# Optimization experiments

Measured on AMD Instinct MI355X. Metric: run time of the kernel, lower is better.

Reference implementation:

```python
import jax, jax.numpy as jnp
import numpy as np

B, L, H, W = 4, 5000, 256, 256
C_IN, DIM_LOI, N_PTS0, N_PTS1, DIM_FC, N_OUT_LINE = 256, 128, 32, 8, 1024, 2500
SCALE = N_PTS0 // N_PTS1  # MaxPool1d kernel/stride


def setup_inputs() -> dict:
    key = jax.random.key(0)
    ks = jax.random.split(key, 8)
    feature = jax.random.normal(ks[0], (B, C_IN, H, W), jnp.float32)
    # line endpoints in pixel coords of the 256x256 feature map
    lines = jax.random.uniform(ks[1], (B, L, 2, 2), jnp.float32) * (H - 1)
    s = lambda fan: 1.0 / np.sqrt(fan)
    fc1_w = (jax.random.normal(ks[2], (DIM_LOI, C_IN), jnp.float32) * s(C_IN))
    fc1_b = jnp.zeros((DIM_LOI,), jnp.float32)
    w1 = jax.random.normal(ks[3], (DIM_LOI * N_PTS1, DIM_FC), jnp.float32) * s(DIM_LOI * N_PTS1)
    b1 = jnp.zeros((DIM_FC,), jnp.float32)
    w2 = jax.random.normal(ks[4], (DIM_FC, DIM_FC), jnp.float32) * s(DIM_FC)
    b2 = jnp.zeros((DIM_FC,), jnp.float32)
    w3 = jax.random.normal(ks[5], (DIM_FC, 4), jnp.float32) * s(DIM_FC)
    b3 = jnp.zeros((4,), jnp.float32)
    return dict(feature=feature, lines=lines, fc1_w=fc1_w, fc1_b=fc1_b,
                w1=w1, b1=b1, w2=w2, b2=b2, w3=w3, b3=b3)


def reference(feature, lines, fc1_w, fc1_b, w1, b1, w2, b2, w3, b3):
    # fc1: 1x1 conv  [B,C_IN,H,W] -> [B,DIM_LOI,H,W]
    x = jnp.einsum('bchw,oc->bohw', feature, fc1_w) + fc1_b[None, :, None, None]

    # sample N_PTS0 points along each line (lerp between endpoints), minus 0.5
    lam = jnp.linspace(0.0, 1.0, N_PTS0, dtype=feature.dtype)[None, None, :, None]
    p = lines[:, :, 0:1, :] * lam + lines[:, :, 1:2, :] * (1.0 - lam) - 0.5  # [B,L,P,2]
    px, py = p[..., 0], p[..., 1]  # px indexes H (rows), py indexes W (cols)
    px0 = jnp.clip(jnp.floor(px), 0.0, H - 1.0)
    py0 = jnp.clip(jnp.floor(py), 0.0, W - 1.0)
    px1 = jnp.clip(px0 + 1.0, 0.0, H - 1.0)
    py1 = jnp.clip(py0 + 1.0, 0.0, W - 1.0)
    ix0, iy0 = px0.astype(jnp.int32), py0.astype(jnp.int32)
    ix1, iy1 = px1.astype(jnp.int32), py1.astype(jnp.int32)
    idx00 = ix0 * W + iy0
    idx10 = ix1 * W + iy0
    idx01 = ix0 * W + iy1
    idx11 = ix1 * W + iy1
    w00 = (px1 - px) * (py1 - py)
    w10 = (px - px0) * (py1 - py)
    w01 = (px1 - px) * (py - py0)
    w11 = (px - px0) * (py - py0)

    def gather_one(fmap, i00, i10, i01, i11, g00, g10, g01, g11):
        f = fmap.reshape(DIM_LOI, H * W)
        g = lambda idx: f[:, idx.reshape(-1)].reshape(DIM_LOI, L, N_PTS0)
        return g(i00) * g00 + g(i10) * g10 + g(i01) * g01 + g(i11) * g11

    xp = jax.vmap(gather_one)(x, idx00, idx10, idx01, idx11, w00, w10, w01, w11)
    # xp: [B, DIM_LOI, L, N_PTS0] -> maxpool along points -> [B, DIM_LOI, L, N_PTS1]
    xp = xp.reshape(B, DIM_LOI, L, N_PTS1, SCALE).max(-1)
    # reshape like torch: [N, DIM_LOI, N_PTS1] -> [N, DIM_LOI*N_PTS1] (channel-major)
    feat = xp.transpose(0, 2, 1, 3).reshape(B, L, DIM_LOI * N_PTS1)

    # fc2 MLP -> 4 logits
    h = jax.nn.relu(feat @ w1 + b1)
    h = jax.nn.relu(h @ w2 + b2)
    logits = h @ w3 + b3  # [B, L, 4]
    s = jax.nn.softmax(logits, axis=-1)

    # threshold conditions
    keep = ((s[..., 1] > 0.25) | (s[..., 2] > 0.25) | (s[..., 3] > 0.25)) & (s[..., 0] < 0.25)

    def select(p0, s0, m):
        cnt = m.sum()
        key = jnp.where(m, jnp.argmax(s0, -1), -1)  # masked-out get -1 -> sorted last
        order = jnp.argsort(-key)  # stable desc sort of argmax class
        idx = order[jnp.arange(N_OUT_LINE) % jnp.maximum(cnt, 1)]
        lo = jnp.where(cnt > 0, p0[idx], 0.0)
        so = jnp.where(cnt > 0, s0[idx], 0.0)
        return lo, so

    lines_out, score_out = jax.vmap(select)(lines, s, keep)
    return lines_out, score_out, s
```

## Files before the change

### kernel.cpp

```cpp
#include <hip/hip_runtime.h>
#include <cstdint>
#include <cstddef>

#define B_     4
#define L_     5000
#define H_     256
#define W_     256
#define HW_    65536
#define CIN_   256
#define DLOI_  128
#define NPTS0_ 32
#define NPTS1_ 8
#define DFC_   1024
#define NOUT_  2500
#define M_     (B_*L_)
#define MPAD_  20096
#define NBAND_ 157

typedef _Float16 f16;
typedef _Float16 f16x4 __attribute__((ext_vector_type(4)));
typedef _Float16 f16x8 __attribute__((ext_vector_type(8)));
typedef float    f32x4 __attribute__((ext_vector_type(4)));

__device__ __forceinline__ void gload16(const void* g, void* l) {
  __builtin_amdgcn_global_load_lds(
      (const __attribute__((address_space(1))) void*)g,
      (__attribute__((address_space(3))) void*)l, 16, 0, 0);
}

__global__ __launch_bounds__(256) void k_wsplit(const float* __restrict__ src,
                                                f16* __restrict__ h,
                                                f16* __restrict__ l) {
  int i = (blockIdx.x * 256 + threadIdx.x) * 4;
  float4 v = *(const float4*)(src + i);
  f16 h0 = (f16)v.x, h1 = (f16)v.y, h2 = (f16)v.z, h3 = (f16)v.w;
  *(f16x4*)(h + i) = (f16x4){h0, h1, h2, h3};
  *(f16x4*)(l + i) = (f16x4){(f16)(v.x - (float)h0), (f16)(v.y - (float)h1),
                             (f16)(v.z - (float)h2), (f16)(v.w - (float)h3)};
}

__global__ __launch_bounds__(1024) void k_order(const float* __restrict__ lines,
                                                int* __restrict__ perm) {
  __shared__ int hist[64];
  __shared__ int off[64];
  const int b = blockIdx.x;
  const int t = threadIdx.x;
  if (t < 64) hist[t] = 0;
  __syncthreads();
  int mycell[5];
  #pragma unroll
  for (int i = 0; i < 5; i++) {
    const int l = t * 5 + i;
    int cell = -1;
    if (l < L_) {
      const float* ln = lines + (size_t)(b * L_ + l) * 4;
      float mx = 0.5f * (ln[0] + ln[2]);
      float my = 0.5f * (ln[1] + ln[3]);
      int cx = min(max((int)mx, 0), 255) >> 5;
      int cy = min(max((int)my, 0), 255) >> 5;
      cell = (cx & 1) | ((cy & 1) << 1) | ((cx & 2) << 1) | ((cy & 2) << 2)
           | ((cx & 4) << 2) | ((cy & 4) << 3);
      atomicAdd(&hist[cell], 1);
    }
    mycell[i] = cell;
  }
  __syncthreads();
  if (t == 0) {
    int s = 0;
    for (int c = 0; c < 64; c++) { off[c] = s; s += hist[c]; }
  }
  __syncthreads();
  #pragma unroll
  for (int i = 0; i < 5; i++) {
    if (mycell[i] >= 0) {
      int slot = atomicAdd(&off[mycell[i]], 1);
      perm[b * L_ + slot] = t * 5 + i;
    }
  }
}

__global__ __launch_bounds__(256) void k_conv_mfma(const float* __restrict__ fin,
                                                   const f16* __restrict__ wh,
                                                   const f16* __restrict__ wl,
                                                   const float* __restrict__ bias,
                                                   float* __restrict__ xout) {
  __shared__ f16 lds[16384];
  const int t = threadIdx.x;
  const int P0 = blockIdx.x * 128;
  const int b  = P0 >> 16;
  const int ph0 = P0 & 65535;
  const int lane = t & 63, wave = t >> 6;
  const int quad = lane >> 4, lo = lane & 15;
  const int wm = wave >> 1, wn = wave & 1;

  const int c_base = (t & 7) * 4;
  const int p = (t >> 3) * 4;
  const size_t fbase = (size_t)b * CIN_ * HW_ + (size_t)ph0 + p;

  const int srow = t >> 2;
  const int skb  = (t & 3) * 16;
  const char* gBh = (const char*)wh + (size_t)srow * 512 + skb;
  const char* gBl = (const char*)wl + (size_t)srow * 512 + skb;
  char* ldsB = (char*)lds + t * 16;

  f32x4 acc[4][4];
  #pragma unroll
  for (int mt = 0; mt < 4; mt++)
    #pragma unroll
    for (int nt = 0; nt < 4; nt++) acc[mt][nt] = (f32x4){0.f, 0.f, 0.f, 0.f};

  float4 av[4], nv[4];
  #pragma unroll
  for (int j = 0; j < 4; j++)
    av[j] = *(const float4*)(fin + fbase + (size_t)(c_base + j) * HW_);

  for (int kc = 0; kc < 8; kc++) {
    const size_t bko = (size_t)kc * 64;
    gload16(gBh + bko,         ldsB + 16384);
    gload16(gBh + 32768 + bko, ldsB + 16384 + 4096);
    gload16(gBl + bko,         ldsB + 24576);
    gload16(gBl + 32768 + bko, ldsB + 24576 + 4096);

    #pragma unroll
    for (int i = 0; i < 4; i++) {
      f16 hh[4], ll[4];
      #pragma unroll
      for (int j = 0; j < 4; j++) {
        float v = ((const float*)&av[j])[i];
        hh[j] = (f16)v;
        ll[j] = (f16)(v - (float)hh[j]);
      }
      *(f16x4*)(&lds[(p + i) * 32 + c_base])        = (f16x4){hh[0], hh[1], hh[2], hh[3]};
      *(f16x4*)(&lds[4096 + (p + i) * 32 + c_base]) = (f16x4){ll[0], ll[1], ll[2], ll[3]};
    }
    __syncthreads();

    if (kc < 7) {
      #pragma unroll
      for (int j = 0; j < 4; j++)
        nv[j] = *(const float4*)(fin + fbase + (size_t)((kc + 1) * 32 + c_base + j) * HW_);
    }

    f16x8 ah[4], al[4], bh4[4], bl4[4];
    #pragma unroll
    for (int mt = 0; mt < 4; mt++) {
      int row = wm * 64 + mt * 16 + lo;
      ah[mt] = *(const f16x8*)(&lds[row * 32 + quad * 8]);
      al[mt] = *(const f16x8*)(&lds[4096 + row * 32 + quad * 8]);
    }
    #pragma unroll
    for (int nt = 0; nt < 4; nt++) {
      int row = wn * 64 + nt * 16 + lo;
      bh4[nt] = *(const f16x8*)(&lds[8192 + row * 32 + quad * 8]);
      bl4[nt] = *(const f16x8*)(&lds[12288 + row * 32 + quad * 8]);
    }
    #pragma unroll
    for (int mt = 0; mt < 4; mt++)
      #pragma unroll
      for (int nt = 0; nt < 4; nt++) {
        acc[mt][nt] = __builtin_amdgcn_mfma_f32_16x16x32_f16(ah[mt], bh4[nt], acc[mt][nt], 0, 0, 0);
        acc[mt][nt] = __builtin_amdgcn_mfma_f32_16x16x32_f16(ah[mt], bl4[nt], acc[mt][nt], 0, 0, 0);
        acc[mt][nt] = __builtin_amdgcn_mfma_f32_16x16x32_f16(al[mt], bh4[nt], acc[mt][nt], 0, 0, 0);
      }
    __syncthreads();
    #pragma unroll
    for (int j = 0; j < 4; j++) av[j] = nv[j];
  }

  #pragma unroll
  for (int nt = 0; nt < 4; nt++) {
    int col = wn * 64 + nt * 16 + lo;
    float bv = bias[col];
    #pragma unroll
    for (int mt = 0; mt < 4; mt++) {
      int rowb = P0 + wm * 64 + mt * 16 + quad * 4;
      #pragma unroll
      for (int r = 0; r < 4; r++)
        xout[(size_t)(rowb + r) * DLOI_ + col] = acc[mt][nt][r] + bv;
    }
  }
}

__global__ __launch_bounds__(128) void k_sample(const float* __restrict__ x,
                                                const float* __restrict__ lines,
                                                const int* __restrict__ perm,
                                                f16* __restrict__ fh,
                                                f16* __restrict__ fl) {
  __shared__ int4   s_off[NPTS0_];
  __shared__ float4 s_wt [NPTS0_];
  const int blk0 = blockIdx.x;
  const int s = (blk0 & 7) * (M_ / 8) + (blk0 >> 3);
  const int b = s / L_;
  const int row = b * L_ + perm[s];
  const int c = threadIdx.x;
  const float* ln = lines + (size_t)row * 4;

  if (c < NPTS0_) {
    const float e0x = ln[0], e0y = ln[1], e1x = ln[2], e1y = ln[3];
    const int i = c;
    float lam = (float)i * (1.0f / 31.0f);
    float px = e0x * lam + e1x * (1.f - lam) - 0.5f;
    float py = e0y * lam + e1y * (1.f - lam) - 0.5f;
    float px0 = fminf(fmaxf(floorf(px), 0.f), 255.f);
    float py0 = fminf(fmaxf(floorf(py), 0.f), 255.f);
    float px1 = fminf(px0 + 1.f, 255.f);
    float py1 = fminf(py0 + 1.f, 255.f);
    int ix0 = (int)px0, iy0 = (int)py0, ix1 = (int)px1, iy1 = (int)py1;
    s_wt[i]  = make_float4((px1 - px) * (py1 - py),
                           (px - px0) * (py1 - py),
                           (px1 - px) * (py - py0),
                           (px - px0) * (py - py0));
    s_off[i] = make_int4((ix0 * W_ + iy0) * (DLOI_ * 4),
                         (ix1 * W_ + iy0) * (DLOI_ * 4),
                         (ix0 * W_ + iy1) * (DLOI_ * 4),
                         (ix1 * W_ + iy1) * (DLOI_ * 4));
  }
  __syncthreads();

  const char* xbc = (const char*)(x + (size_t)b * HW_ * DLOI_) + c * 4;
  f16x8 vh, vl;
  for (int q = 0; q < NPTS1_; q++) {
    float m = -1e30f;
    #pragma unroll
    for (int r = 0; r < 4; r++) {
      const int i = q * 4 + r;
      const int4   o = s_off[i];
      const float4 w = s_wt[i];
      float v = w.x * *(const float*)(xbc + o.x)
              + w.y * *(const float*)(xbc + o.y)
              + w.z * *(const float*)(xbc + o.z)
              + w.w * *(const float*)(xbc + o.w);
      m = fmaxf(m, v);
    }
    f16 h = (f16)m;
    vh[q] = h;
    vl[q] = (f16)(m - (float)h);
  }
  *(f16x8*)(fh + (size_t)row * DFC_ + c * 8) = vh;
  *(f16x8*)(fl + (size_t)row * DFC_ + c * 8) = vl;
}

__global__ __launch_bounds__(256) void k_tsplit(const float* __restrict__ Wsrc,
                                                f16* __restrict__ Th,
                                                f16* __restrict__ Tl) {
  __shared__ float tile[32][33];
  const int bj = blockIdx.x, bi = blockIdx.y;
  const int tx = threadIdx.x & 31, ty = threadIdx.x >> 5;
  #pragma unroll
  for (int r = ty; r < 32; r += 8)
    tile[r][tx] = Wsrc[(size_t)(bi * 32 + r) * 1024 + bj * 32 + tx];
  __syncthreads();
  #pragma unroll
  for (int r = ty; r < 32; r += 8) {
    float v = tile[tx][r];
    f16 h = (f16)v;
    size_t o = (size_t)(bj * 32 + r) * 1024 + bi * 32 + tx;
    Th[o] = h;
    Tl[o] = (f16)(v - (float)h);
  }
}

#define BKT_    32
#define NTT_    (DFC_/BKT_)
#define SLOT_B_ 49152
#define AH_O_   0
#define AL_O_   8192
#define BH_O_   16384
#define BL_O_   32768

template <bool SPLIT_OUT>
__global__ __launch_bounds__(512, 2) void k_gemm_f16x3(
    const f16* __restrict__ Ah, const f16* __restrict__ Al,
    const f16* __restrict__ Bh, const f16* __restrict__ Bl,
    const float* __restrict__ bias,
    f16* __restrict__ Oh, f16* __restrict__ Ol,
    const float* __restrict__ w3, float* __restrict__ part) {
  __shared__ f16 lds[3 * SLOT_B_ / 2];
  char* ldsc = (char*)lds;

  const int orig = blockIdx.x;
  const int xcd = orig & 7, bidx = orig >> 3;
  const int qq = 628 >> 3, rr = 628 & 7;
  const int wg = (xcd < rr ? xcd * (qq + 1) : rr * (qq + 1) + (xcd - rr) * qq) + bidx;
  const int band = wg >> 2;
  const int nb   = wg & 3;
  const int r0 = band * 128;
  const int n0 = nb * 256;

  const int t = threadIdx.x;
  const int lane = t & 63, wave = t >> 6;
  const int quad = lane >> 4, lo = lane & 15;
  const int wm = wave >> 2, wn = wave & 3;

  const uint32_t usA  = (uint32_t)t ^ (((uint32_t)t >> 3) & 7);
  const uint32_t uB1  = (uint32_t)t + 512u;
  const uint32_t usB1 = uB1 ^ ((uB1 >> 3) & 7);
  const size_t sA  = (size_t)(usA  >> 2) * 2048 + (size_t)(usA  & 3) * 16;
  const size_t sB1 = (size_t)(usB1 >> 2) * 2048 + (size_t)(usB1 & 3) * 16;

  const char* gAh  = (const char*)Ah + (size_t)r0 * 2048 + sA;
  const char* gAl  = (const char*)Al + (size_t)r0 * 2048 + sA;
  const char* gBh0 = (const char*)Bh + (size_t)n0 * 2048 + sA;
  const char* gBh1 = (const char*)Bh + (size_t)n0 * 2048 + sB1;
  const char* gBl0 = (const char*)Bl + (size_t)n0 * 2048 + sA;
  const char* gBl1 = (const char*)Bl + (size_t)n0 * 2048 + sB1;

  const int dAh  = AH_O_ + t * 16;
  const int dAl  = AL_O_ + t * 16;
  const int dBh0 = BH_O_ + t * 16;
  const int dBh1 = BH_O_ + 8192 + t * 16;
  const int dBl0 = BL_O_ + t * 16;
  const int dBl1 = BL_O_ + 8192 + t * 16;

  int roffA[4], roffB[4];
  #pragma unroll
  for (int mt = 0; mt < 4; mt++) {
    int r = wm * 64 + mt * 16 + lo;
    roffA[mt] = (((r * 4 + quad) ^ ((r >> 1) & 7)) << 4);
  }
  #pragma unroll
  for (int nt = 0; nt < 4; nt++) {
    int r = wn * 64 + nt * 16 + lo;
    roffB[nt] = (((r * 4 + quad) ^ ((r >> 1) & 7)) << 4);
  }

  f32x4 acc[4][4];
  #pragma unroll
  for (int mt = 0; mt < 4; mt++)
    #pragma unroll
    for (int nt = 0; nt < 4; nt++) acc[mt][nt] = (f32x4){0.f, 0.f, 0.f, 0.f};

  gload16(gAh,        ldsc + dAh);
  gload16(gAl,        ldsc + dAl);
  gload16(gBh0,       ldsc + dBh0);
  gload16(gBh1,       ldsc + dBh1);
  gload16(gBl0,       ldsc + dBl0);
  gload16(gBl1,       ldsc + dBl1);
  gload16(gAh  + 64,  ldsc + SLOT_B_ + dAh);
  gload16(gAl  + 64,  ldsc + SLOT_B_ + dAl);
  gload16(gBh0 + 64,  ldsc + SLOT_B_ + dBh0);
  gload16(gBh1 + 64,  ldsc + SLOT_B_ + dBh1);
  gload16(gBl0 + 64,  ldsc + SLOT_B_ + dBl0);
  gload16(gBl1 + 64,  ldsc + SLOT_B_ + dBl1);
  asm volatile("s_waitcnt vmcnt(6)" ::: "memory");
  __builtin_amdgcn_s_barrier();

  int cur = 0, stg = 2;
  for (int tt = 0; tt < NTT_; ++tt) {
    const char* sc = ldsc + cur * SLOT_B_;
    char* sw = ldsc + stg * SLOT_B_;
    const size_t go = (size_t)tt * 64 + 128;
    const bool pf = (tt + 2 < NTT_);

    if (pf) {
      gload16(gAh  + go, sw + dAh);
      gload16(gAl  + go, sw + dAl);
      gload16(gBh0 + go, sw + dBh0);
      gload16(gBh1 + go, sw + dBh1);
      gload16(gBl0 + go, sw + dBl0);
      gload16(gBl1 + go, sw + dBl1);
    }

    f16x8 ah[4], bh[4], al[4], bl[4];
    #pragma unroll
    for (int mt = 0; mt < 4; mt++)
      ah[mt] = *(const f16x8*)(sc + AH_O_ + roffA[mt]);
    #pragma unroll
    for (int nt = 0; nt < 4; nt++)
      bh[nt] = *(const f16x8*)(sc + BH_O_ + roffB[nt]);
    #pragma unroll
    for (int mt = 0; mt < 4; mt++)
      al[mt] = *(const f16x8*)(sc + AL_O_ + roffA[mt]);
    #pragma unroll
    for (int nt = 0; nt < 4; nt++)
      bl[nt] = *(const f16x8*)(sc + BL_O_ + roffB[nt]);

    __builtin_amdgcn_s_setprio(1);
    #pragma unroll
    for (int mt = 0; mt < 4; mt++)
      #pragma unroll
      for (int nt = 0; nt < 4; nt++)
        acc[mt][nt] = __builtin_amdgcn_mfma_f32_16x16x32_f16(ah[mt], bh[nt], acc[mt][nt], 0, 0, 0);
    #pragma unroll
    for (int mt = 0; mt < 4; mt++)
      #pragma unroll
      for (int nt = 0; nt < 4; nt++)
        acc[mt][nt] = __builtin_amdgcn_mfma_f32_16x16x32_f16(al[mt], bh[nt], acc[mt][nt], 0, 0, 0);
    #pragma unroll
    for (int mt = 0; mt < 4; mt++)
      #pragma unroll
      for (int nt = 0; nt < 4; nt++)
        acc[mt][nt] = __builtin_amdgcn_mfma_f32_16x16x32_f16(ah[mt], bl[nt], acc[mt][nt], 0, 0, 0);
    __builtin_amdgcn_s_setprio(0);

    if (tt < NTT_ - 2)       asm volatile("s_waitcnt vmcnt(6)" ::: "memory");
    else if (tt == NTT_ - 2) asm volatile("s_waitcnt vmcnt(0)" ::: "memory");
    __builtin_amdgcn_s_barrier();

    cur = (cur == 2) ? 0 : cur + 1;
    stg = (stg == 2) ? 0 : stg + 1;
  }

  if (SPLIT_OUT) {
    char* ep = ldsc + wave * 16384;
    #pragma unroll
    for (int mt = 0; mt < 4; mt++)
      #pragma unroll
      for (int nt = 0; nt < 4; nt++) {
        const int col = n0 + wn * 64 + nt * 16 + lo;
        const float bv = bias[col];
        const int col_l = nt * 16 + lo;
        #pragma unroll
        for (int r = 0; r < 4; r++) {
          const int rl = mt * 16 + quad * 4 + r;
          float v = fmaxf(acc[mt][nt][r] + bv, 0.f);
          f16 h = (f16)v;
          f16 lw = (f16)(v - (float)h);
          const int byte = rl * 128 + ((((col_l >> 3) ^ (rl & 7)) << 4)) + (col_l & 7) * 2;
          *(f16*)(ep + byte) = h;
          *(f16*)(ep + 8192 + byte) = lw;
        }
      }
    asm volatile("s_waitcnt lgkmcnt(0)" ::: "memory");
    __builtin_amdgcn_sched_barrier(0);
    const int r8 = lane >> 3;
    const int ck = lane & 7;
    #pragma unroll
    for (int g = 0; g < 8; g++) {
      const int rl = g * 8 + r8;
      const int grow = r0 + wm * 64 + rl;
      const int swz = ((ck ^ (rl & 7)) << 4);
      f16x8 vh = *(const f16x8*)(ep + rl * 128 + swz);
      f16x8 vl = *(const f16x8*)(ep + 8192 + rl * 128 + swz);
      if (grow < M_) {
        const size_t gb = (size_t)grow * 2048 + (size_t)(n0 + wn * 64) * 2 + ck * 16;
        *(f16x8*)((char*)Oh + gb) = vh;
        *(f16x8*)((char*)Ol + gb) = vl;
      }
    }
  } else {
    const int slot = nb * 4 + wn;
    #pragma unroll
    for (int mt = 0; mt < 4; mt++) {
      float p[4][4];
      #pragma unroll
      for (int r = 0; r < 4; r++)
        #pragma unroll
        for (int j = 0; j < 4; j++) p[r][j] = 0.f;
      #pragma unroll
      for (int nt = 0; nt < 4; nt++) {
        const int col = n0 + wn * 64 + nt * 16 + lo;
        const float bv = bias[col];
        float4 wv = *(const float4*)(w3 + col * 4);
        #pragma unroll
        for (int r = 0; r < 4; r++) {
          float v = fmaxf(acc[mt][nt][r] + bv, 0.f);
          p[r][0] = fmaf(v, wv.x, p[r][0]);
          p[r][1] = fmaf(v, wv.y, p[r][1]);
          p[r][2] = fmaf(v, wv.z, p[r][2]);
          p[r][3] = fmaf(v, wv.w, p[r][3]);
        }
      }
      #pragma unroll
      for (int r = 0; r < 4; r++)
        #pragma unroll
        for (int j = 0; j < 4; j++) {
          p[r][j] += __shfl_xor(p[r][j], 1);
          p[r][j] += __shfl_xor(p[r][j], 2);
          p[r][j] += __shfl_xor(p[r][j], 4);
          p[r][j] += __shfl_xor(p[r][j], 8);
        }
      if (lo == 0) {
        const int rowb = r0 + wm * 64 + mt * 16 + quad * 4;
        #pragma unroll
        for (int r = 0; r < 4; r++)
          *(float4*)(part + ((size_t)slot * MPAD_ + rowb + r) * 4) =
              make_float4(p[r][0], p[r][1], p[r][2], p[r][3]);
      }
    }
  }
}

__global__ __launch_bounds__(256) void k_head2(const float* __restrict__ part,
                                               const float* __restrict__ b3,
                                               float* __restrict__ s_out,
                                               int* __restrict__ key_out) {
  const int row = blockIdx.x * 256 + threadIdx.x;
  if (row >= M_) return;
  float l0 = b3[0], l1 = b3[1], l2 = b3[2], l3 = b3[3];
  #pragma unroll
  for (int sl = 0; sl < 16; sl++) {
    float4 p = *(const float4*)(part + ((size_t)sl * MPAD_ + row) * 4);
    l0 += p.x; l1 += p.y; l2 += p.z; l3 += p.w;
  }
  float mx = fmaxf(fmaxf(l0, l1), fmaxf(l2, l3));
  float e0 = expf(l0 - mx), e1 = expf(l1 - mx), e2 = expf(l2 - mx), e3 = expf(l3 - mx);
  float inv = 1.f / (e0 + e1 + e2 + e3);
  float s0 = e0 * inv, s1 = e1 * inv, s2 = e2 * inv, s3 = e3 * inv;
  *(float4*)(s_out + (size_t)row * 4) = make_float4(s0, s1, s2, s3);
  bool keep = ((s1 > 0.25f) || (s2 > 0.25f) || (s3 > 0.25f)) && (s0 < 0.25f);
  int am = 0; float best = s0;
  if (s1 > best) { best = s1; am = 1; }
  if (s2 > best) { best = s2; am = 2; }
  if (s3 > best) { best = s3; am = 3; }
  key_out[row] = keep ? am : -1;
}

__global__ __launch_bounds__(1024) void k_select(const int* __restrict__ key,
                                                 const float* __restrict__ lines,
                                                 const float* __restrict__ s,
                                                 float* __restrict__ out_lines,
                                                 float* __restrict__ out_score) {
  __shared__ int s_ord[L_];
  __shared__ int s_scan[1024];
  __shared__ int s_tot[5];
  const int b = blockIdx.x;
  const int t = threadIdx.x;
  const int base_l = t * 5;
  int cls[5];
  int c[5] = {0, 0, 0, 0, 0};
  #pragma unroll
  for (int i = 0; i < 5; i++) {
    int l = base_l + i;
    int cl = -1;
    if (l < L_) {
      int k = key[b * L_ + l];
      cl = (k < 0) ? 4 : (3 - k);
      c[cl]++;
    }
    cls[i] = cl;
  }
  int pf[5];
  for (int cc = 0; cc < 5; cc++) {
    s_scan[t] = c[cc];
    __syncthreads();
    for (int off = 1; off < 1024; off <<= 1) {
      int add = (t >= off) ? s_scan[t - off] : 0;
      __syncthreads();
      s_scan[t] += add;
      __syncthreads();
    }
    pf[cc] = s_scan[t] - c[cc];
    if (t == 1023) s_tot[cc] = s_scan[1023];
    __syncthreads();
  }
  int basec[5];
  basec[0] = 0;
  #pragma unroll
  for (int cc = 1; cc < 5; cc++) basec[cc] = basec[cc - 1] + s_tot[cc - 1];
  int run[5] = {0, 0, 0, 0, 0};
  #pragma unroll
  for (int i = 0; i < 5; i++) {
    if (cls[i] >= 0) {
      int cl = cls[i];
      int pos = basec[cl] + pf[cl] + run[cl];
      run[cl]++;
      s_ord[pos] = base_l + i;
    }
  }
  const int cnt = L_ - s_tot[4];
  __syncthreads();
  for (int j = t; j < NOUT_; j += 1024) {
    float4 lv = make_float4(0.f, 0.f, 0.f, 0.f);
    float4 sv = make_float4(0.f, 0.f, 0.f, 0.f);
    if (cnt > 0) {
      int idx = s_ord[j % cnt];
      lv = *(const float4*)(lines + (size_t)(b * L_ + idx) * 4);
      sv = *(const float4*)(s + (size_t)(b * L_ + idx) * 4);
    }
    *(float4*)(out_lines + (size_t)(b * NOUT_ + j) * 4) = lv;
    *(float4*)(out_score + (size_t)(b * NOUT_ + j) * 4) = sv;
  }
}

extern "C" void kernel_launch(void* const* d_in, const int* in_sizes, int n_in,
                              void* d_out, int out_size, void* d_ws, size_t ws_size,
                              hipStream_t stream) {
  const float* feature = (const float*)d_in[0];
  const float* lines   = (const float*)d_in[1];
  const float* fc1_w   = (const float*)d_in[2];
  const float* fc1_b   = (const float*)d_in[3];
  const float* w1      = (const float*)d_in[4];
  const float* b1      = (const float*)d_in[5];
  const float* w2      = (const float*)d_in[6];
  const float* b2      = (const float*)d_in[7];
  const float* w3      = (const float*)d_in[8];
  const float* b3      = (const float*)d_in[9];

  float* out_lines = (float*)d_out;
  float* out_score = out_lines + B_ * NOUT_ * 4;
  float* s_out     = out_score + B_ * NOUT_ * 4;

  char* ws = (char*)d_ws;
  float* x    = (float*)(ws);
  f16*   h1h  = (f16*)(ws);
  f16*   h1l  = (f16*)(ws + 41156608ull);
  float* part = (float*)(ws + 82313216ull);
  f16*   fh   = (f16*)(ws + 134217728ull);
  f16*   fl   = (f16*)(ws + 134217728ull + 41156608ull);
  f16*   wt1h = (f16*)(ws + 216530944ull);
  f16*   wt1l = (f16*)(ws + 216530944ull + 2097152ull);
  f16*   wt2h = (f16*)(ws + 216530944ull + 2ull * 2097152ull);
  f16*   wt2l = (f16*)(ws + 216530944ull + 3ull * 2097152ull);
  int*   keys = (int*)(ws + 224919552ull);
  f16*   wc_h = (f16*)(ws + 224999552ull);
  f16*   wc_l = (f16*)(ws + 224999552ull + 65536ull);

  k_order<<<dim3(B_), 1024, 0, stream>>>(lines, keys);
  k_wsplit<<<dim3(32), 256, 0, stream>>>(fc1_w, wc_h, wc_l);
  k_tsplit<<<dim3(32, 32), 256, 0, stream>>>(w1, wt1h, wt1l);
  k_tsplit<<<dim3(32, 32), 256, 0, stream>>>(w2, wt2h, wt2l);
  k_conv_mfma<<<dim3((B_ * HW_) / 128), 256, 0, stream>>>(feature, wc_h, wc_l, fc1_b, x);
  k_sample<<<dim3(M_), 128, 0, stream>>>(x, lines, keys, fh, fl);
  k_gemm_f16x3<true><<<dim3(628), 512, 0, stream>>>(
      fh, fl, wt1h, wt1l, b1, h1h, h1l, nullptr, nullptr);
  k_gemm_f16x3<false><<<dim3(628), 512, 0, stream>>>(
      h1h, h1l, wt2h, wt2l, b2, nullptr, nullptr, w3, part);
  k_head2<<<dim3((M_ + 255) / 256), 256, 0, stream>>>(part, b3, s_out, keys);
  k_select<<<dim3(B_), 1024, 0, stream>>>(keys, lines, s_out, out_lines, out_score);
}
```

Baseline: 870.5 us.

## Shrink split-f16 GEMM tile to 128x128 with 256 threads and double buffering

Reworks the two split-precision MLP GEMMs to use 128x128 output tiles per 256-thread workgroup instead of 128x256 per 512 threads. This doubles the grid to 1256 blocks and cuts LDS from a three-slot to a two-slot pipeline (64KB). It also simplifies the XCD-aware block remap and the w3 partial-slot indexing. The aim is more resident workgroups and better load balance across CUs, at the cost of less B-tile reuse per block, more global traffic, and a shallower prefetch that waits on vmcnt(0) every iteration.

```diff
diff --git a/kernel.cpp b/kernel.cpp
--- a/kernel.cpp
+++ b/kernel.cpp
@@ -262,55 +262,48 @@
 
 #define BKT_    32
 #define NTT_    (DFC_/BKT_)
-#define SLOT_B_ 49152
+#define SLOT_B_ 32768
 #define AH_O_   0
 #define AL_O_   8192
 #define BH_O_   16384
-#define BL_O_   32768
+#define BL_O_   24576
 
 template <bool SPLIT_OUT>
-__global__ __launch_bounds__(512, 2) void k_gemm_f16x3(
+__global__ __launch_bounds__(256, 2) void k_gemm_f16x3(
     const f16* __restrict__ Ah, const f16* __restrict__ Al,
     const f16* __restrict__ Bh, const f16* __restrict__ Bl,
     const float* __restrict__ bias,
     f16* __restrict__ Oh, f16* __restrict__ Ol,
     const float* __restrict__ w3, float* __restrict__ part) {
-  __shared__ f16 lds[3 * SLOT_B_ / 2];
+  __shared__ f16 lds[2 * SLOT_B_ / 2];
   char* ldsc = (char*)lds;
 
   const int orig = blockIdx.x;
-  const int xcd = orig & 7, bidx = orig >> 3;
-  const int qq = 628 >> 3, rr = 628 & 7;
-  const int wg = (xcd < rr ? xcd * (qq + 1) : rr * (qq + 1) + (xcd - rr) * qq) + bidx;
-  const int band = wg >> 2;
-  const int nb   = wg & 3;
+  const int wg = (orig & 7) * 157 + (orig >> 3);
+  const int band = wg >> 3;
+  const int nb   = wg & 7;
   const int r0 = band * 128;
-  const int n0 = nb * 256;
+  const int n0 = nb * 128;
 
   const int t = threadIdx.x;
   const int lane = t & 63, wave = t >> 6;
   const int quad = lane >> 4, lo = lane & 15;
-  const int wm = wave >> 2, wn = wave & 3;
-
-  const uint32_t usA  = (uint32_t)t ^ (((uint32_t)t >> 3) & 7);
-  const uint32_t uB1  = (uint32_t)t + 512u;
-  const uint32_t usB1 = uB1 ^ ((uB1 >> 3) & 7);
-  const size_t sA  = (size_t)(usA  >> 2) * 2048 + (size_t)(usA  & 3) * 16;
-  const size_t sB1 = (size_t)(usB1 >> 2) * 2048 + (size_t)(usB1 & 3) * 16;
-
-  const char* gAh  = (const char*)Ah + (size_t)r0 * 2048 + sA;
-  const char* gAl  = (const char*)Al + (size_t)r0 * 2048 + sA;
-  const char* gBh0 = (const char*)Bh + (size_t)n0 * 2048 + sA;
-  const char* gBh1 = (const char*)Bh + (size_t)n0 * 2048 + sB1;
-  const char* gBl0 = (const char*)Bl + (size_t)n0 * 2048 + sA;
-  const char* gBl1 = (const char*)Bl + (size_t)n0 * 2048 + sB1;
-
-  const int dAh  = AH_O_ + t * 16;
-  const int dAl  = AL_O_ + t * 16;
-  const int dBh0 = BH_O_ + t * 16;
-  const int dBh1 = BH_O_ + 8192 + t * 16;
-  const int dBl0 = BL_O_ + t * 16;
-  const int dBl1 = BL_O_ + 8192 + t * 16;
+  const int wm = wave >> 1, wn = wave & 1;
+
+  const uint32_t u0 = (uint32_t)t;
+  const uint32_t u1 = (uint32_t)t + 256u;
+  const uint32_t us0 = u0 ^ ((u0 >> 3) & 7);
+  const uint32_t us1 = u1 ^ ((u1 >> 3) & 7);
+  const size_t s0 = (size_t)(us0 >> 2) * 2048 + (size_t)(us0 & 3) * 16;
+  const size_t s1 = (size_t)(us1 >> 2) * 2048 + (size_t)(us1 & 3) * 16;
+
+  const char* gAh = (const char*)Ah + (size_t)r0 * 2048;
+  const char* gAl = (const char*)Al + (size_t)r0 * 2048;
+  const char* gBh = (const char*)Bh + (size_t)n0 * 2048;
+  const char* gBl = (const char*)Bl + (size_t)n0 * 2048;
+
+  const int d0 = t * 16;
+  const int d1 = 4096 + t * 16;
 
   int roffA[4], roffB[4];
   #pragma unroll
@@ -330,35 +323,32 @@
     #pragma unroll
     for (int nt = 0; nt < 4; nt++) acc[mt][nt] = (f32x4){0.f, 0.f, 0.f, 0.f};
 
-  gload16(gAh,        ldsc + dAh);
-  gload16(gAl,        ldsc + dAl);
-  gload16(gBh0,       ldsc + dBh0);
-  gload16(gBh1,       ldsc + dBh1);
-  gload16(gBl0,       ldsc + dBl0);
-  gload16(gBl1,       ldsc + dBl1);
-  gload16(gAh  + 64,  ldsc + SLOT_B_ + dAh);
-  gload16(gAl  + 64,  ldsc + SLOT_B_ + dAl);
-  gload16(gBh0 + 64,  ldsc + SLOT_B_ + dBh0);
-  gload16(gBh1 + 64,  ldsc + SLOT_B_ + dBh1);
-  gload16(gBl0 + 64,  ldsc + SLOT_B_ + dBl0);
-  gload16(gBl1 + 64,  ldsc + SLOT_B_ + dBl1);
-  asm volatile("s_waitcnt vmcnt(6)" ::: "memory");
+  gload16(gAh + s0, ldsc + AH_O_ + d0);
+  gload16(gAh + s1, ldsc + AH_O_ + d1);
+  gload16(gAl + s0, ldsc + AL_O_ + d0);
+  gload16(gAl + s1, ldsc + AL_O_ + d1);
+  gload16(gBh + s0, ldsc + BH_O_ + d0);
+  gload16(gBh + s1, ldsc + BH_O_ + d1);
+  gload16(gBl + s0, ldsc + BL_O_ + d0);
+  gload16(gBl + s1, ldsc + BL_O_ + d1);
+  asm volatile("s_waitcnt vmcnt(0)" ::: "memory");
   __builtin_amdgcn_s_barrier();
 
-  int cur = 0, stg = 2;
   for (int tt = 0; tt < NTT_; ++tt) {
-    const char* sc = ldsc + cur * SLOT_B_;
-    char* sw = ldsc + stg * SLOT_B_;
-    const size_t go = (size_t)tt * 64 + 128;
-    const bool pf = (tt + 2 < NTT_);
+    const char* sc = ldsc + (tt & 1) * SLOT_B_;
+    char* sw = ldsc + ((tt + 1) & 1) * SLOT_B_;
+    const size_t go = (size_t)(tt + 1) * 64;
+    const bool pf = (tt + 1 < NTT_);
 
     if (pf) {
-      gload16(gAh  + go, sw + dAh);
-      gload16(gAl  + go, sw + dAl);
-      gload16(gBh0 + go, sw + dBh0);
-      gload16(gBh1 + go, sw + dBh1);
-      gload16(gBl0 + go, sw + dBl0);
-      gload16(gBl1 + go, sw + dBl1);
+      gload16(gAh + go + s0, sw + AH_O_ + d0);
+      gload16(gAh + go + s1, sw + AH_O_ + d1);
+      gload16(gAl + go + s0, sw + AL_O_ + d0);
+      gload16(gAl + go + s1, sw + AL_O_ + d1);
+      gload16(gBh + go + s0, sw + BH_O_ + d0);
+      gload16(gBh + go + s1, sw + BH_O_ + d1);
+      gload16(gBl + go + s0, sw + BL_O_ + d0);
+      gload16(gBl + go + s1, sw + BL_O_ + d1);
     }
 
     f16x8 ah[4], bh[4], al[4], bl[4];
@@ -393,12 +383,8 @@
         acc[mt][nt] = __builtin_amdgcn_mfma_f32_16x16x32_f16(ah[mt], bl[nt], acc[mt][nt], 0, 0, 0);
     __builtin_amdgcn_s_setprio(0);
 
-    if (tt < NTT_ - 2)       asm volatile("s_waitcnt vmcnt(6)" ::: "memory");
-    else if (tt == NTT_ - 2) asm volatile("s_waitcnt vmcnt(0)" ::: "memory");
+    if (pf) asm volatile("s_waitcnt vmcnt(0)" ::: "memory");
     __builtin_amdgcn_s_barrier();
-
-    cur = (cur == 2) ? 0 : cur + 1;
-    stg = (stg == 2) ? 0 : stg + 1;
   }
 
   if (SPLIT_OUT) {
@@ -439,7 +425,7 @@
       }
     }
   } else {
-    const int slot = nb * 4 + wn;
+    const int slot = nb * 2 + wn;
     #pragma unroll
     for (int mt = 0; mt < 4; mt++) {
       float p[4][4];
@@ -612,9 +598,9 @@
   k_tsplit<<<dim3(32, 32), 256, 0, stream>>>(w2, wt2h, wt2l);
   k_conv_mfma<<<dim3((B_ * HW_) / 128), 256, 0, stream>>>(feature, wc_h, wc_l, fc1_b, x);
   k_sample<<<dim3(M_), 128, 0, stream>>>(x, lines, keys, fh, fl);
-  k_gemm_f16x3<true><<<dim3(628), 512, 0, stream>>>(
+  k_gemm_f16x3<true><<<dim3(1256), 256, 0, stream>>>(
       fh, fl, wt1h, wt1l, b1, h1h, h1l, nullptr, nullptr);
-  k_gemm_f16x3<false><<<dim3(628), 512, 0, stream>>>(
+  k_gemm_f16x3<false><<<dim3(1256), 256, 0, stream>>>(
       h1h, h1l, wt2h, wt2l, b2, nullptr, nullptr, w3, part);
   k_head2<<<dim3((M_ + 255) / 256), 256, 0, stream>>>(part, b3, s_out, keys);
   k_select<<<dim3(B_), 1024, 0, stream>>>(keys, lines, s_out, out_lines, out_score);
```

After: 827.1 us (median of 2 runs). -5.0%, faster.
